# Performance work log

Measured on AMD Instinct MI355X. Metric: run time of the kernel, lower is better.

The kernel has to match this reference:

```python
import jax, jax.numpy as jnp
import numpy as np

N, C, E, H = 50000, 128, 1_600_000, 32
JITTER = 1e-20


def _lin(k, fan_in, fan_out):
    return jax.random.normal(k, (fan_in, fan_out), jnp.float32) / np.sqrt(fan_in)


def setup_inputs() -> dict:
    key = jax.random.key(0)
    ks = jax.random.split(key, 20)
    x = jax.random.normal(ks[0], (N, C), jnp.float32)
    edge_index = jax.random.randint(ks[1], (2, E), 0, N, dtype=jnp.int64)
    inp = {"x": x, "edge_index": edge_index}
    # actor params
    inp["aW"] = _lin(ks[2], C, C); inp["ab"] = jnp.zeros((C,), jnp.float32)
    inp["a1W"] = _lin(ks[3], C, H); inp["a1b"] = jnp.zeros((H,), jnp.float32)
    inp["a2W"] = _lin(ks[4], H, H); inp["a2b"] = jnp.zeros((H,), jnp.float32)
    inp["a3W"] = _lin(ks[5], H, 2); inp["a3b"] = jnp.zeros((2,), jnp.float32)
    # critic params
    inp["cW"] = _lin(ks[6], C, C); inp["cb"] = jnp.zeros((C,), jnp.float32)
    inp["c1W"] = _lin(ks[7], C, H); inp["c1b"] = jnp.zeros((H,), jnp.float32)
    inp["c2W"] = _lin(ks[8], H, H); inp["c2b"] = jnp.zeros((H,), jnp.float32)
    inp["c3W"] = _lin(ks[9], H, 2); inp["c3b"] = jnp.zeros((2,), jnp.float32)
    return inp


def gcn_conv(x, src, dst, W, b):
    """Standard PyG GCNConv: add self-loops, symmetric degree norm, X@W, scatter-add, +bias."""
    n = x.shape[0]
    loop = jnp.arange(n)
    s = jnp.concatenate([src, loop])  # [E+N]
    d = jnp.concatenate([dst, loop])
    deg = jax.ops.segment_sum(jnp.ones_like(d, jnp.float32), d, num_segments=n)
    dinv = jnp.where(deg > 0, jax.lax.rsqrt(deg), 0.0)
    norm = dinv[s] * dinv[d]                     # [E+N]
    h = x @ W                                    # [N, C]
    agg = jax.ops.segment_sum(h[s] * norm[:, None], d, num_segments=n)
    return agg + b


def reference(x, edge_index, aW, ab, a1W, a1b, a2W, a2b, a3W, a3b,
              cW, cb, c1W, c1b, c2W, c2b, c3W, c3b):
    src, dst = edge_index[0], edge_index[1]
    # actor
    h = jax.nn.relu(gcn_conv(x, src, dst, aW, ab)) + x
    h = jax.nn.relu(h @ a1W + a1b)
    h = jax.nn.relu(h @ a2W + a2b)
    a = h @ a3W + a3b                            # [N, 2]
    concentration = jax.nn.softplus(a[:, 0]) + JITTER
    p = jax.nn.softplus(a[:, 1])
    action2_probs = p / jnp.sum(p)
    # critic
    hc = jax.nn.relu(gcn_conv(x, src, dst, cW, cb)) + x
    hc = jnp.sum(hc, axis=0)                     # [C]
    hc = jax.nn.relu(hc @ c1W + c1b)
    hc = jax.nn.relu(hc @ c2W + c2b)
    value = hc @ c3W + c3b                       # [2]
    return (concentration, value, action2_probs)
```

## Files before the change

kernel.cpp:

```cpp
#include <hip/hip_runtime.h>
#include <hip/hip_bf16.h>
#include <hip/hip_fp16.h>
#include <math.h>

#define C 128
#define BCAP 12288

using half8x = __attribute__((ext_vector_type(8))) _Float16;
using half4x = __attribute__((ext_vector_type(4))) _Float16;
using f32x4  = __attribute__((ext_vector_type(4))) float;

__device__ inline float4 h4_to_f4(uint2 u) {
    __half2 p0 = *(__half2*)&u.x;
    __half2 p1 = *(__half2*)&u.y;
    float2 f0 = __half22float2(p0), f1 = __half22float2(p1);
    return make_float4(f0.x, f0.y, f1.x, f1.y);
}

__device__ inline float softplusf(float v) {
    return (v > 20.f) ? v : log1pf(expf(v));
}

__global__ __launch_bounds__(256) void initk(unsigned* gcur, float* colsum, float* pSum) {
    int t = threadIdx.x;
    gcur[t] = 0u;
    if (t < 128) colsum[t] = 0.f;
    if (t == 128) pSum[0] = 0.f;
}

__global__ __launch_bounds__(256) void bink(const int* __restrict__ ei,
                                            unsigned* __restrict__ gcur,
                                            unsigned* __restrict__ gstage,
                                            int E, int NBKT) {
    __shared__ unsigned raw[6400];
    __shared__ unsigned image[6400];
    __shared__ unsigned cnt[256];
    __shared__ unsigned pref[256];
    __shared__ unsigned cur[256];
    __shared__ unsigned gb[256];
    int t = threadIdx.x, b = blockIdx.x;
    int elo = (int)((long long)b * E / 256);
    int ehi = (int)((long long)(b + 1) * E / 256);
    int n = ehi - elo;

    for (int i = t; i < n; i += 256) {
        int d = __builtin_nontemporal_load(ei + E + elo + i);
        int s = __builtin_nontemporal_load(ei + elo + i);
        raw[i] = (unsigned)s | ((unsigned)(d & 255) << 16) | ((unsigned)(d >> 8) << 24);
    }
    cnt[t] = 0u; cur[t] = 0u;
    __syncthreads();
    for (int i = t; i < n; i += 256) atomicAdd(&cnt[raw[i] >> 24], 1u);
    __syncthreads();
    pref[t] = cnt[t];
    __syncthreads();
    for (int off = 1; off < 256; off <<= 1) {
        unsigned add = (t >= off) ? pref[t - off] : 0u;
        __syncthreads();
        pref[t] += add;
        __syncthreads();
    }
    gb[t] = (t < NBKT && cnt[t]) ? atomicAdd(&gcur[t], cnt[t]) : 0u;
    __syncthreads();
    for (int i = t; i < n; i += 256) {
        unsigned v = raw[i];
        unsigned B = v >> 24;
        unsigned pos = (pref[B] - cnt[B]) + atomicAdd(&cur[B], 1u);
        image[pos] = v & 0xFFFFFFu;
    }
    __syncthreads();
    int wv = t >> 6, lane = t & 63;
    for (int B = wv; B < NBKT; B += 4) {
        unsigned c = cnt[B];
        if (!c) continue;
        unsigned eb = pref[B] - c;
        unsigned gbase = gb[B];
        unsigned c2 = (gbase < BCAP) ? ((c < BCAP - gbase) ? c : BCAP - gbase) : 0u;
        for (unsigned i = lane; i < c2; i += 64)
            gstage[(size_t)B * BCAP + gbase + i] = image[eb + i];
    }
}

__global__ void bktscank(const unsigned* __restrict__ gcur, unsigned* __restrict__ bktbase, int NBKT) {
    __shared__ unsigned tmp[256];
    int t = threadIdx.x;
    unsigned g = (t < NBKT) ? gcur[t] : 0u;
    unsigned v = (g < BCAP) ? g : BCAP;
    tmp[t] = v;
    __syncthreads();
    for (int off = 1; off < 256; off <<= 1) {
        unsigned add = (t >= off) ? tmp[t - off] : 0u;
        __syncthreads();
        tmp[t] += add;
        __syncthreads();
    }
    if (t < NBKT) bktbase[t] = tmp[t] - v;
}

__global__ __launch_bounds__(256) void placek(const unsigned* __restrict__ gstage,
                                              const unsigned* __restrict__ gcur,
                                              const unsigned* __restrict__ bktbase,
                                              int* __restrict__ rowptr, float* __restrict__ dinv,
                                              int* __restrict__ col, int N, int NBKT) {
    __shared__ unsigned image[BCAP];
    __shared__ unsigned cnt[256];
    __shared__ unsigned pref[256];
    __shared__ unsigned cur[256];
    int B = blockIdx.x, t = threadIdx.x;
    unsigned g = gcur[B];
    unsigned m = (g < BCAP) ? g : BCAP;
    unsigned base = bktbase[B];
    const unsigned* st = gstage + (size_t)B * BCAP;

    cnt[t] = 0u; cur[t] = 0u;
    __syncthreads();
    for (unsigned i = t; i < m; i += 256) atomicAdd(&cnt[(st[i] >> 16) & 255u], 1u);
    __syncthreads();
    pref[t] = cnt[t];
    __syncthreads();
    for (int off = 1; off < 256; off <<= 1) {
        unsigned add = (t >= off) ? pref[t - off] : 0u;
        __syncthreads();
        pref[t] += add;
        __syncthreads();
    }
    int d = B * 256 + t;
    if (d < N) {
        rowptr[d] = (int)(base + pref[t] - cnt[t]);
        dinv[d] = rsqrtf((float)(cnt[t] + 1u));
    }
    if (B == NBKT - 1 && t == 0) rowptr[N] = (int)(base + m);
    for (unsigned i = t; i < m; i += 256) {
        unsigned v = st[i];
        unsigned dl = (v >> 16) & 255u;
        unsigned pos = (pref[dl] - cnt[dl]) + atomicAdd(&cur[dl], 1u);
        image[pos] = v & 0xFFFFu;
    }
    __syncthreads();
    for (unsigned i = t; i < m; i += 256) col[base + i] = (int)image[i];
}

__global__ __launch_bounds__(256) void xhk(const float* __restrict__ x, const float* __restrict__ dinv,
                                           __half* __restrict__ xh, int N) {
    int i = blockIdx.x * 256 + threadIdx.x;
    if (i >= N * 64) return;
    int node = i >> 6, fp = (i & 63) * 2;
    float w = dinv[node];
    float2 f = *(const float2*)&x[(size_t)node * C + fp];
    __half2 h = __floats2half2_rn(f.x * w, f.y * w);
    *(unsigned*)&xh[(size_t)node * C + fp] = *(unsigned*)&h;
}

__global__ __launch_bounds__(256) void gatherk(const int* __restrict__ col,
                                               const int* __restrict__ rowptr,
                                               const __half* __restrict__ xh,
                                               const float* __restrict__ dinv,
                                               __half* __restrict__ gg, int N) {
    __shared__ int snb[4][64];
    int t = threadIdx.x;
    int wid = t >> 6, lane = t & 63;
    int d = blockIdx.x * 4 + wid;
    if (d >= N) return;
    int beg = rowptr[d], end = rowptr[d + 1];
    int half = lane >> 5, sub = lane & 31;
    int f = sub * 4;

    float a0 = 0.f, a1 = 0.f, a2 = 0.f, a3 = 0.f;

    for (int c = beg; c < end; c += 64) {
        if (c + lane < end) snb[wid][lane] = col[c + lane];
        int n = end - c; if (n > 64) n = 64;
        int j = 0;
        for (; j + 3 < n; j += 4) {
            size_t i0 = (size_t)snb[wid][j + half] * C + f;
            size_t i1 = (size_t)snb[wid][j + 2 + half] * C + f;
            float4 v0 = h4_to_f4(*(const uint2*)&xh[i0]);
            float4 v1 = h4_to_f4(*(const uint2*)&xh[i1]);
            a0 += v0.x + v1.x;
            a1 += v0.y + v1.y;
            a2 += v0.z + v1.z;
            a3 += v0.w + v1.w;
        }
        for (; j < n; j += 2) {
            if (j + half < n) {
                float4 v = h4_to_f4(*(const uint2*)&xh[(size_t)snb[wid][j + half] * C + f]);
                a0 += v.x; a1 += v.y; a2 += v.z; a3 += v.w;
            }
        }
    }
    a0 += __shfl_xor(a0, 32, 64);
    a1 += __shfl_xor(a1, 32, 64);
    a2 += __shfl_xor(a2, 32, 64);
    a3 += __shfl_xor(a3, 32, 64);

    if (half == 0) {
        float4 s4 = h4_to_f4(*(const uint2*)&xh[(size_t)d * C + f]);
        float dv = dinv[d];
        __half2 h0 = __floats2half2_rn((a0 + s4.x) * dv, (a1 + s4.y) * dv);
        __half2 h1 = __floats2half2_rn((a2 + s4.z) * dv, (a3 + s4.w) * dv);
        uint2 u; u.x = *(unsigned*)&h0; u.y = *(unsigned*)&h1;
        *(uint2*)&gg[(size_t)d * C + f] = u;
    }
}

__global__ __launch_bounds__(256) void gemm2k(const __half* __restrict__ gg,
                                              const float* __restrict__ aW,
                                              const float* __restrict__ cW,
                                              const float* __restrict__ ab,
                                              const float* __restrict__ cb,
                                              const float* __restrict__ x,
                                              const float* __restrict__ a1W, const float* __restrict__ a1b,
                                              const float* __restrict__ a2W, const float* __restrict__ a2b,
                                              const float* __restrict__ a3W, const float* __restrict__ a3b,
                                              float* __restrict__ scratch,
                                              float* __restrict__ out, float* __restrict__ pSum, int N) {
    __shared__ char As[32768];
    __shared__ char Bs[32768];
    const bool actor = (blockIdx.y == 0);
    const float* W = actor ? aW : cW;
    const float* bias = actor ? ab : cb;
    const int row0 = blockIdx.x * 128;
    const int t = threadIdx.x;

#pragma unroll
    for (int i = 0; i < 8; ++i) {
        int c = t + i * 256;
        int row = c >> 4, cb16 = (c & 15) * 16;
        int grow = row0 + row;
        uint4 u = make_uint4(0u, 0u, 0u, 0u);
        if (grow < N) u = *(const uint4*)&gg[(size_t)grow * C + (c & 15) * 8];
        *(uint4*)(As + row * 256 + (cb16 ^ ((row & 7) << 4))) = u;
    }
    {
        int kb = (t & 31) * 4;
#pragma unroll
        for (int ni = 0; ni < 4; ++ni) {
            int n0 = ni * 32 + (t >> 5) * 4;
            float wr[4][4];
#pragma unroll
            for (int i = 0; i < 4; ++i)
                *(float4*)&wr[i][0] = *(const float4*)&W[(size_t)(kb + i) * C + n0];
#pragma unroll
            for (int j = 0; j < 4; ++j) {
                int n = n0 + j;
                half4x h = { (_Float16)wr[0][j], (_Float16)wr[1][j], (_Float16)wr[2][j], (_Float16)wr[3][j] };
                *(half4x*)(Bs + n * 256 + ((kb * 2) ^ ((n & 7) << 4))) = h;
            }
        }
    }
    __syncthreads();

    int wv = t >> 6, l = t & 63;
    int lm = l & 15, lk = l >> 4;
    int koffB = lk * 16;

    half8x af[2][4];
#pragma unroll
    for (int r = 0; r < 2; ++r) {
        int row = wv * 32 + r * 16 + lm;
        const char* rp = As + row * 256;
        int sw = (row & 7) << 4;
#pragma unroll
        for (int kc = 0; kc < 4; ++kc)
            af[r][kc] = *(const half8x*)(rp + ((kc * 64 + koffB) ^ sw));
    }
    __syncthreads();

    float csum[8];
#pragma unroll
    for (int nc = 0; nc < 8; ++nc) csum[nc] = 0.f;

#pragma unroll
    for (int nc = 0; nc < 8; ++nc) {
        int n = nc * 16 + lm;
        const char* np = Bs + n * 256;
        int swn = (n & 7) << 4;
        half8x bf[4];
#pragma unroll
        for (int kc = 0; kc < 4; ++kc)
            bf[kc] = *(const half8x*)(np + ((kc * 64 + koffB) ^ swn));
        float bsv = bias[n];
#pragma unroll
        for (int r = 0; r < 2; ++r) {
            f32x4 acc = {0.f, 0.f, 0.f, 0.f};
#pragma unroll
            for (int kc = 0; kc < 4; ++kc)
                acc = __builtin_amdgcn_mfma_f32_16x16x32_f16(af[r][kc], bf[kc], acc, 0, 0, 0);
            int grl0 = wv * 32 + r * 16 + lk * 4;
#pragma unroll
            for (int j = 0; j < 4; ++j) {
                int rowL = grl0 + j;
                int grow = row0 + rowL;
                float v = 0.f;
                if (grow < N) v = fmaxf(acc[j] + bsv, 0.f) + x[(size_t)grow * C + n];
                if (actor) {
                    *(_Float16*)(As + rowL * 256 + ((n * 2) ^ ((rowL & 7) << 4))) = (_Float16)v;
                } else {
                    csum[nc] += v;
                }
            }
        }
    }
    __syncthreads();

    if (actor) {
        _Float16* w2t = (_Float16*)(Bs + 8192);
        _Float16* h1b = (_Float16*)(Bs + 10752);
        _Float16* h2b = (_Float16*)(Bs + 20992);
        float* w3s = (float*)(Bs + 31232);
        float* b1s = (float*)(Bs + 31488);
        float* b2s = (float*)(Bs + 31616);
        float* b3s = (float*)(Bs + 31744);
        for (int idx = t; idx < 4096; idx += 256) {
            int k = idx >> 5, n = idx & 31;
            *(_Float16*)(Bs + n * 256 + ((k * 2) ^ ((n & 7) << 4))) = (_Float16)a1W[idx];
        }
        for (int idx = t; idx < 1024; idx += 256) {
            int k = idx >> 5, n = idx & 31;
            w2t[n * 40 + k] = (_Float16)a2W[idx];
        }
        if (t < 64) w3s[t] = a3W[t];
        if (t < 32) b1s[t] = a1b[t];
        else if (t < 64) b2s[t - 32] = a2b[t - 32];
        else if (t < 66) b3s[t - 64] = a3b[t - 64];
        __syncthreads();

#pragma unroll
        for (int rt = 0; rt < 2; ++rt) {
            int rowA = wv * 32 + rt * 16 + lm;
            const char* rp = As + rowA * 256;
            int swA = (rowA & 7) << 4;
            half8x a1f[4];
#pragma unroll
            for (int kc = 0; kc < 4; ++kc)
                a1f[kc] = *(const half8x*)(rp + ((kc * 64 + koffB) ^ swA));
#pragma unroll
            for (int ct = 0; ct < 2; ++ct) {
                int n = ct * 16 + lm;
                int swn = (n & 7) << 4;
                f32x4 acc1 = {0.f, 0.f, 0.f, 0.f};
#pragma unroll
                for (int kc = 0; kc < 4; ++kc) {
                    half8x bq = *(const half8x*)(Bs + n * 256 + ((kc * 64 + koffB) ^ swn));
                    acc1 = __builtin_amdgcn_mfma_f32_16x16x32_f16(a1f[kc], bq, acc1, 0, 0, 0);
                }
                float bv = b1s[n];
#pragma unroll
                for (int j = 0; j < 4; ++j) {
                    int node = rt * 16 + lk * 4 + j;
                    h1b[(wv * 32 + node) * 40 + n] = (_Float16)fmaxf(acc1[j] + bv, 0.f);
                }
            }
        }
#pragma unroll
        for (int rt = 0; rt < 2; ++rt) {
            half8x a2f = *(const half8x*)(h1b + (wv * 32 + rt * 16 + lm) * 40 + lk * 8);
#pragma unroll
            for (int ct = 0; ct < 2; ++ct) {
                int n = ct * 16 + lm;
                half8x b2f = *(const half8x*)(w2t + n * 40 + lk * 8);
                f32x4 acc2 = {0.f, 0.f, 0.f, 0.f};
                acc2 = __builtin_amdgcn_mfma_f32_16x16x32_f16(a2f, b2f, acc2, 0, 0, 0);
                float bv = b2s[n];
#pragma unroll
                for (int j = 0; j < 4; ++j) {
                    int node = rt * 16 + lk * 4 + j;
                    h2b[(wv * 32 + node) * 40 + n] = (_Float16)fmaxf(acc2[j] + bv, 0.f);
                }
            }
        }
        {
            int nl = l >> 1, o = l & 1;
            float acc3 = b3s[o];
            const _Float16* hrow = h2b + (wv * 32 + nl) * 40;
#pragma unroll
            for (int k = 0; k < 32; ++k) acc3 += (float)hrow[k] * w3s[k * 2 + o];
            int node = row0 + wv * 32 + nl;
            float spv = 0.f;
            if (node < N) {
                spv = softplusf(acc3);
                if (o == 0) out[node] = spv + 1e-20f;
                else out[(size_t)N + 2 + node] = spv;
            }
            float pv = (o == 1) ? spv : 0.f;
            pv += __shfl_xor(pv, 1, 64);
            pv += __shfl_xor(pv, 2, 64);
            pv += __shfl_xor(pv, 4, 64);
            pv += __shfl_xor(pv, 8, 64);
            pv += __shfl_xor(pv, 16, 64);
            pv += __shfl_xor(pv, 32, 64);
            if (l == 0) atomicAdd(pSum, pv);
        }
    } else {
        float* scol = (float*)Bs;
#pragma unroll
        for (int nc = 0; nc < 8; ++nc) {
            float v = csum[nc];
            v += __shfl_xor(v, 16, 64);
            v += __shfl_xor(v, 32, 64);
            if (lk == 0) scol[wv * 128 + nc * 16 + lm] = v;
        }
        __syncthreads();
        if (t < 128)
            scratch[(size_t)blockIdx.x * 128 + t] = scol[t] + scol[128 + t] + scol[256 + t] + scol[384 + t];
    }
}

__global__ __launch_bounds__(128) void csredk(const float* __restrict__ scratch, float* __restrict__ colsum, int nblk) {
    int t = threadIdx.x;
    float s = 0.f;
    for (int b = blockIdx.x; b < nblk; b += gridDim.x)
        s += scratch[(size_t)b * 128 + t];
    atomicAdd(&colsum[t], s);
}

__global__ void critick(const float* __restrict__ colsum,
                        const float* __restrict__ c1W, const float* __restrict__ c1b,
                        const float* __restrict__ c2W, const float* __restrict__ c2b,
                        const float* __restrict__ c3W, const float* __restrict__ c3b,
                        float* __restrict__ out, int N) {
    __shared__ float s1[32], s2[32];
    int t = threadIdx.x;
    if (t < 32) {
        float acc = c1b[t];
        for (int k = 0; k < 128; ++k) acc += colsum[k] * c1W[k * 32 + t];
        s1[t] = fmaxf(acc, 0.f);
    }
    __syncthreads();
    if (t < 32) {
        float acc = c2b[t];
        for (int k = 0; k < 32; ++k) acc += s1[k] * c2W[k * 32 + t];
        s2[t] = fmaxf(acc, 0.f);
    }
    __syncthreads();
    if (t < 2) {
        float acc = c3b[t];
        for (int k = 0; k < 32; ++k) acc += s2[k] * c3W[k * 2 + t];
        out[(size_t)N + t] = acc;
    }
}

__global__ __launch_bounds__(256) void normk(float* __restrict__ out, const float* __restrict__ pSum, int N) {
    int i = blockIdx.x * 256 + threadIdx.x;
    if (i < N) out[(size_t)N + 2 + i] /= pSum[0];
}

extern "C" void kernel_launch(void* const* d_in, const int* in_sizes, int n_in,
                              void* d_out, int out_size, void* d_ws, size_t ws_size,
                              hipStream_t stream) {
    const float* x   = (const float*)d_in[0];
    const int* ei    = (const int*)d_in[1];
    const float* aW  = (const float*)d_in[2];
    const float* ab  = (const float*)d_in[3];
    const float* a1W = (const float*)d_in[4];
    const float* a1b = (const float*)d_in[5];
    const float* a2W = (const float*)d_in[6];
    const float* a2b = (const float*)d_in[7];
    const float* a3W = (const float*)d_in[8];
    const float* a3b = (const float*)d_in[9];
    const float* cW  = (const float*)d_in[10];
    const float* cb  = (const float*)d_in[11];
    const float* c1W = (const float*)d_in[12];
    const float* c1b = (const float*)d_in[13];
    const float* c2W = (const float*)d_in[14];
    const float* c2b = (const float*)d_in[15];
    const float* c3W = (const float*)d_in[16];
    const float* c3b = (const float*)d_in[17];

    const int N = in_sizes[0] / C;
    const int E = in_sizes[1] / 2;
    const int NBKT = (N + 255) / 256;
    const int nblkx = (N + 127) / 128;
    float* out = (float*)d_out;

    char* ws = (char*)d_ws;
    size_t off = 0;
    auto alloc = [&](size_t bytes) {
        size_t o = off;
        off = (off + bytes + 255) & ~(size_t)255;
        return (void*)(ws + o);
    };
    unsigned* gcur    = (unsigned*)alloc(256 * 4);
    unsigned* bktbase = (unsigned*)alloc(256 * 4);
    unsigned* gstage  = (unsigned*)alloc((size_t)NBKT * BCAP * 4);
    int* rowptr       = (int*)alloc((size_t)(N + 1) * 4);
    float* dinv       = (float*)alloc((size_t)N * 4);
    int* colidx       = (int*)alloc((size_t)E * 4);
    __half* xh        = (__half*)alloc((size_t)N * C * 2);
    __half* gg        = (__half*)alloc((size_t)N * C * 2);
    float* scratch    = (float*)alloc((size_t)nblkx * 128 * 4);
    float* colsum     = (float*)alloc(128 * 4);
    float* pSum       = (float*)alloc(4);

    initk<<<1, 256, 0, stream>>>(gcur, colsum, pSum);
    bink<<<256, 256, 0, stream>>>(ei, gcur, gstage, E, NBKT);
    bktscank<<<1, 256, 0, stream>>>(gcur, bktbase, NBKT);
    placek<<<NBKT, 256, 0, stream>>>(gstage, gcur, bktbase, rowptr, dinv, colidx, N, NBKT);
    xhk<<<(N * 64 + 255) / 256, 256, 0, stream>>>(x, dinv, xh, N);
    gatherk<<<(N + 3) / 4, 256, 0, stream>>>(colidx, rowptr, xh, dinv, gg, N);
    gemm2k<<<dim3(nblkx, 2), 256, 0, stream>>>(gg, aW, cW, ab, cb, x,
                                               a1W, a1b, a2W, a2b, a3W, a3b,
                                               scratch, out, pSum, N);
    csredk<<<8, 128, 0, stream>>>(scratch, colsum, nblkx);
    critick<<<1, 64, 0, stream>>>(colsum, c1W, c1b, c2W, c2b, c3W, c3b, out, N);
    normk<<<(N + 255) / 256, 256, 0, stream>>>(out, pSum, N);
}
```

Measured before the change: 210.3 us.

## Pre-transpose weights to fp16 once and trim gemm2k LDS staging

```diff
diff --git a/kernel.cpp b/kernel.cpp
--- a/kernel.cpp
+++ b/kernel.cpp
@@ -26,6 +26,22 @@
     gcur[t] = 0u;
     if (t < 128) colsum[t] = 0.f;
     if (t == 128) pSum[0] = 0.f;
+}
+
+__global__ __launch_bounds__(256) void wtk(const float* __restrict__ aW, const float* __restrict__ cW,
+                                           const float* __restrict__ a1W,
+                                           __half* __restrict__ wt, __half* __restrict__ a1wt) {
+    int idx = blockIdx.x * 256 + threadIdx.x;
+    if (idx < 32768) {
+        int y = idx >> 14, r = idx & 16383;
+        int k = r >> 7, n = r & 127;
+        const float* W = y ? cW : aW;
+        wt[((size_t)y << 14) + n * 128 + k] = __float2half(W[k * 128 + n]);
+    } else if (idx < 36864) {
+        int r = idx - 32768;
+        int k = r >> 5, n = r & 31;
+        a1wt[n * 128 + k] = __float2half(a1W[k * 32 + n]);
+    }
 }
 
 __global__ __launch_bounds__(256) void bink(const int* __restrict__ ei,
@@ -141,14 +157,16 @@
 }
 
 __global__ __launch_bounds__(256) void xhk(const float* __restrict__ x, const float* __restrict__ dinv,
-                                           __half* __restrict__ xh, int N) {
+                                           __half* __restrict__ xh, __half* __restrict__ x16, int N) {
     int i = blockIdx.x * 256 + threadIdx.x;
     if (i >= N * 64) return;
     int node = i >> 6, fp = (i & 63) * 2;
     float w = dinv[node];
     float2 f = *(const float2*)&x[(size_t)node * C + fp];
     __half2 h = __floats2half2_rn(f.x * w, f.y * w);
+    __half2 hx = __floats2half2_rn(f.x, f.y);
     *(unsigned*)&xh[(size_t)node * C + fp] = *(unsigned*)&h;
+    *(unsigned*)&x16[(size_t)node * C + fp] = *(unsigned*)&hx;
 }
 
 __global__ __launch_bounds__(256) void gatherk(const int* __restrict__ col,
@@ -204,23 +222,26 @@
 }
 
 __global__ __launch_bounds__(256) void gemm2k(const __half* __restrict__ gg,
-                                              const float* __restrict__ aW,
-                                              const float* __restrict__ cW,
-                                              const float* __restrict__ ab,
-                                              const float* __restrict__ cb,
-                                              const float* __restrict__ x,
-                                              const float* __restrict__ a1W, const float* __restrict__ a1b,
+                                              const __half* __restrict__ wt,
+                                              const __half* __restrict__ a1wt,
+                                              const float* __restrict__ ab, const float* __restrict__ cb,
+                                              const __half* __restrict__ x16,
+                                              const float* __restrict__ a1b,
                                               const float* __restrict__ a2W, const float* __restrict__ a2b,
                                               const float* __restrict__ a3W, const float* __restrict__ a3b,
                                               float* __restrict__ scratch,
                                               float* __restrict__ out, float* __restrict__ pSum, int N) {
     __shared__ char As[32768];
-    __shared__ char Bs[32768];
+    __shared__ char Aux[13312];
     const bool actor = (blockIdx.y == 0);
-    const float* W = actor ? aW : cW;
     const float* bias = actor ? ab : cb;
+    const __half* W = wt + (actor ? 0 : 16384);
     const int row0 = blockIdx.x * 128;
     const int t = threadIdx.x;
+
+    _Float16* w2t = (_Float16*)Aux;
+    _Float16* h1b = (_Float16*)(Aux + 2560);
+    float* w3s    = (float*)(Aux + 12800);
 
 #pragma unroll
     for (int i = 0; i < 8; ++i) {
@@ -231,28 +252,21 @@
         if (grow < N) u = *(const uint4*)&gg[(size_t)grow * C + (c & 15) * 8];
         *(uint4*)(As + row * 256 + (cb16 ^ ((row & 7) << 4))) = u;
     }
-    {
-        int kb = (t & 31) * 4;
-#pragma unroll
-        for (int ni = 0; ni < 4; ++ni) {
-            int n0 = ni * 32 + (t >> 5) * 4;
-            float wr[4][4];
-#pragma unroll
-            for (int i = 0; i < 4; ++i)
-                *(float4*)&wr[i][0] = *(const float4*)&W[(size_t)(kb + i) * C + n0];
-#pragma unroll
-            for (int j = 0; j < 4; ++j) {
-                int n = n0 + j;
-                half4x h = { (_Float16)wr[0][j], (_Float16)wr[1][j], (_Float16)wr[2][j], (_Float16)wr[3][j] };
-                *(half4x*)(Bs + n * 256 + ((kb * 2) ^ ((n & 7) << 4))) = h;
-            }
-        }
+    if (actor) {
+#pragma unroll
+        for (int i = 0; i < 4; ++i) {
+            int idx = t + i * 256;
+            int k = idx >> 5, n = idx & 31;
+            w2t[n * 40 + k] = (_Float16)a2W[idx];
+        }
+        if (t < 64) w3s[t] = a3W[t];
     }
     __syncthreads();
 
     int wv = t >> 6, l = t & 63;
     int lm = l & 15, lk = l >> 4;
     int koffB = lk * 16;
+    int koffH = lk * 8;
 
     half8x af[2][4];
 #pragma unroll
@@ -264,7 +278,6 @@
         for (int kc = 0; kc < 4; ++kc)
             af[r][kc] = *(const half8x*)(rp + ((kc * 64 + koffB) ^ sw));
     }
-    __syncthreads();
 
     float csum[8];
 #pragma unroll
@@ -273,12 +286,11 @@
 #pragma unroll
     for (int nc = 0; nc < 8; ++nc) {
         int n = nc * 16 + lm;
-        const char* np = Bs + n * 256;
-        int swn = (n & 7) << 4;
+        const __half* wp = W + n * 128;
         half8x bf[4];
 #pragma unroll
         for (int kc = 0; kc < 4; ++kc)
-            bf[kc] = *(const half8x*)(np + ((kc * 64 + koffB) ^ swn));
+            bf[kc] = *(const half8x*)(wp + kc * 32 + koffH);
         float bsv = bias[n];
 #pragma unroll
         for (int r = 0; r < 2; ++r) {
@@ -292,7 +304,7 @@
                 int rowL = grl0 + j;
                 int grow = row0 + rowL;
                 float v = 0.f;
-                if (grow < N) v = fmaxf(acc[j] + bsv, 0.f) + x[(size_t)grow * C + n];
+                if (grow < N) v = fmaxf(acc[j] + bsv, 0.f) + __half2float(x16[(size_t)grow * C + n]);
                 if (actor) {
                     *(_Float16*)(As + rowL * 256 + ((n * 2) ^ ((rowL & 7) << 4))) = (_Float16)v;
                 } else {
@@ -304,27 +316,6 @@
     __syncthreads();
 
     if (actor) {
-        _Float16* w2t = (_Float16*)(Bs + 8192);
-        _Float16* h1b = (_Float16*)(Bs + 10752);
-        _Float16* h2b = (_Float16*)(Bs + 20992);
-        float* w3s = (float*)(Bs + 31232);
-        float* b1s = (float*)(Bs + 31488);
-        float* b2s = (float*)(Bs + 31616);
-        float* b3s = (float*)(Bs + 31744);
-        for (int idx = t; idx < 4096; idx += 256) {
-            int k = idx >> 5, n = idx & 31;
-            *(_Float16*)(Bs + n * 256 + ((k * 2) ^ ((n & 7) << 4))) = (_Float16)a1W[idx];
-        }
-        for (int idx = t; idx < 1024; idx += 256) {
-            int k = idx >> 5, n = idx & 31;
-            w2t[n * 40 + k] = (_Float16)a2W[idx];
-        }
-        if (t < 64) w3s[t] = a3W[t];
-        if (t < 32) b1s[t] = a1b[t];
-        else if (t < 64) b2s[t - 32] = a2b[t - 32];
-        else if (t < 66) b3s[t - 64] = a3b[t - 64];
-        __syncthreads();
-
 #pragma unroll
         for (int rt = 0; rt < 2; ++rt) {
             int rowA = wv * 32 + rt * 16 + lm;
@@ -337,62 +328,70 @@
 #pragma unroll
             for (int ct = 0; ct < 2; ++ct) {
                 int n = ct * 16 + lm;
-                int swn = (n & 7) << 4;
+                const __half* ap = a1wt + n * 128;
                 f32x4 acc1 = {0.f, 0.f, 0.f, 0.f};
 #pragma unroll
                 for (int kc = 0; kc < 4; ++kc) {
-                    half8x bq = *(const half8x*)(Bs + n * 256 + ((kc * 64 + koffB) ^ swn));
+                    half8x bq = *(const half8x*)(ap + kc * 32 + koffH);
                     acc1 = __builtin_amdgcn_mfma_f32_16x16x32_f16(a1f[kc], bq, acc1, 0, 0, 0);
                 }
-                float bv = b1s[n];
+                float bv = a1b[n];
+#pragma unroll
+                for (int j = 0; j < 4; ++j)
+                    h1b[(wv * 32 + rt * 16 + lk * 4 + j) * 40 + n] = (_Float16)fmaxf(acc1[j] + bv, 0.f);
+            }
+        }
+
+        float wave_psum = 0.f;
+        float b30 = a3b[0], b31 = a3b[1];
+#pragma unroll
+        for (int rt = 0; rt < 2; ++rt) {
+            int rowH = wv * 32 + rt * 16 + lm;
+            half4x alo = *(const half4x*)(h1b + rowH * 40 + koffH);
+            half4x ahi = *(const half4x*)(h1b + rowH * 40 + koffH + 4);
+            half8x a2f = __builtin_shufflevector(alo, ahi, 0, 1, 2, 3, 4, 5, 6, 7);
+            float p0[4] = {0.f, 0.f, 0.f, 0.f}, p1[4] = {0.f, 0.f, 0.f, 0.f};
+#pragma unroll
+            for (int ct = 0; ct < 2; ++ct) {
+                int n = ct * 16 + lm;
+                half4x blo = *(const half4x*)(w2t + n * 40 + koffH);
+                half4x bhi = *(const half4x*)(w2t + n * 40 + koffH + 4);
+                half8x b2f = __builtin_shufflevector(blo, bhi, 0, 1, 2, 3, 4, 5, 6, 7);
+                f32x4 acc2 = {0.f, 0.f, 0.f, 0.f};
+                acc2 = __builtin_amdgcn_mfma_f32_16x16x32_f16(a2f, b2f, acc2, 0, 0, 0);
+                float bv = a2b[n];
+                float w30 = w3s[n * 2], w31 = w3s[n * 2 + 1];
 #pragma unroll
                 for (int j = 0; j < 4; ++j) {
-                    int node = rt * 16 + lk * 4 + j;
-                    h1b[(wv * 32 + node) * 40 + n] = (_Float16)fmaxf(acc1[j] + bv, 0.f);
+                    float h2v = fmaxf(acc2[j] + bv, 0.f);
+                    p0[j] += h2v * w30;
+                    p1[j] += h2v * w31;
                 }
             }
-        }
-#pragma unroll
-        for (int rt = 0; rt < 2; ++rt) {
-            half8x a2f = *(const half8x*)(h1b + (wv * 32 + rt * 16 + lm) * 40 + lk * 8);
-#pragma unroll
-            for (int ct = 0; ct < 2; ++ct) {
-                int n = ct * 16 + lm;
-                half8x b2f = *(const half8x*)(w2t + n * 40 + lk * 8);
-                f32x4 acc2 = {0.f, 0.f, 0.f, 0.f};
-                acc2 = __builtin_amdgcn_mfma_f32_16x16x32_f16(a2f, b2f, acc2, 0, 0, 0);
-                float bv = b2s[n];
-#pragma unroll
-                for (int j = 0; j < 4; ++j) {
-                    int node = rt * 16 + lk * 4 + j;
-                    h2b[(wv * 32 + node) * 40 + n] = (_Float16)fmaxf(acc2[j] + bv, 0.f);
+#pragma unroll
+            for (int j = 0; j < 4; ++j) {
+                float q0 = p0[j], q1 = p1[j];
+                q0 += __shfl_xor(q0, 1, 64); q0 += __shfl_xor(q0, 2, 64);
+                q0 += __shfl_xor(q0, 4, 64); q0 += __shfl_xor(q0, 8, 64);
+                q1 += __shfl_xor(q1, 1, 64); q1 += __shfl_xor(q1, 2, 64);
+                q1 += __shfl_xor(q1, 4, 64); q1 += __shfl_xor(q1, 8, 64);
+                if (lm == 0) {
+                    int node = row0 + wv * 32 + rt * 16 + lk * 4 + j;
+                    if (node < N) {
+                        float s0 = softplusf(q0 + b30);
+                        float s1 = softplusf(q1 + b31);
+                        out[node] = s0 + 1e-20f;
+                        out[(size_t)N + 2 + node] = s1;
+                        wave_psum += s1;
+                    }
                 }
             }
         }
-        {
-            int nl = l >> 1, o = l & 1;
-            float acc3 = b3s[o];
-            const _Float16* hrow = h2b + (wv * 32 + nl) * 40;
-#pragma unroll
-            for (int k = 0; k < 32; ++k) acc3 += (float)hrow[k] * w3s[k * 2 + o];
-            int node = row0 + wv * 32 + nl;
-            float spv = 0.f;
-            if (node < N) {
-                spv = softplusf(acc3);
-                if (o == 0) out[node] = spv + 1e-20f;
-                else out[(size_t)N + 2 + node] = spv;
-            }
-            float pv = (o == 1) ? spv : 0.f;
-            pv += __shfl_xor(pv, 1, 64);
-            pv += __shfl_xor(pv, 2, 64);
-            pv += __shfl_xor(pv, 4, 64);
-            pv += __shfl_xor(pv, 8, 64);
-            pv += __shfl_xor(pv, 16, 64);
-            pv += __shfl_xor(pv, 32, 64);
-            if (l == 0) atomicAdd(pSum, pv);
-        }
+        wave_psum += __shfl_xor(wave_psum, 16, 64);
+        wave_psum += __shfl_xor(wave_psum, 32, 64);
+        if (l == 0) atomicAdd(pSum, wave_psum);
     } else {
-        float* scol = (float*)Bs;
+        float* scol = (float*)Aux;
 #pragma unroll
         for (int nc = 0; nc < 8; ++nc) {
             float v = csum[nc];
@@ -487,19 +486,23 @@
     float* dinv       = (float*)alloc((size_t)N * 4);
     int* colidx       = (int*)alloc((size_t)E * 4);
     __half* xh        = (__half*)alloc((size_t)N * C * 2);
+    __half* x16       = (__half*)alloc((size_t)N * C * 2);
     __half* gg        = (__half*)alloc((size_t)N * C * 2);
+    __half* wt        = (__half*)alloc(2 * 16384 * 2);
+    __half* a1wt      = (__half*)alloc(4096 * 2);
     float* scratch    = (float*)alloc((size_t)nblkx * 128 * 4);
     float* colsum     = (float*)alloc(128 * 4);
     float* pSum       = (float*)alloc(4);
 
     initk<<<1, 256, 0, stream>>>(gcur, colsum, pSum);
+    wtk<<<144, 256, 0, stream>>>(aW, cW, a1W, wt, a1wt);
     bink<<<256, 256, 0, stream>>>(ei, gcur, gstage, E, NBKT);
     bktscank<<<1, 256, 0, stream>>>(gcur, bktbase, NBKT);
     placek<<<NBKT, 256, 0, stream>>>(gstage, gcur, bktbase, rowptr, dinv, colidx, N, NBKT);
-    xhk<<<(N * 64 + 255) / 256, 256, 0, stream>>>(x, dinv, xh, N);
+    xhk<<<(N * 64 + 255) / 256, 256, 0, stream>>>(x, dinv, xh, x16, N);
     gatherk<<<(N + 3) / 4, 256, 0, stream>>>(colidx, rowptr, xh, dinv, gg, N);
-    gemm2k<<<dim3(nblkx, 2), 256, 0, stream>>>(gg, aW, cW, ab, cb, x,
-                                               a1W, a1b, a2W, a2b, a3W, a3b,
+    gemm2k<<<dim3(nblkx, 2), 256, 0, stream>>>(gg, wt, a1wt, ab, cb, x16,
+                                               a1b, a2W, a2b, a3W, a3b,
                                                scratch, out, pSum, N);
     csredk<<<8, 128, 0, stream>>>(scratch, colsum, nblkx);
     critick<<<1, 64, 0, stream>>>(colsum, c1W, c1b, c2W, c2b, c3W, c3b, out, N);
```

Result: faster. 204.2 us (-2.9%).
